# Kernel optimization log

Measured on AMD Instinct MI355X. Metric: run time of the kernel, lower is better.

The kernel has to match this reference:

```python
import jax, jax.numpy as jnp
import numpy as np
from jax import lax

B, T, V, E, H = 256, 16, 32000, 256, 512


def setup_inputs() -> dict:
    key = jax.random.key(0)
    ks = jax.random.split(key, 10)
    s = 0.02
    return {
        "x": jax.random.normal(ks[0], (B, E), dtype=jnp.float32),
        "bb_w": jax.random.normal(ks[1], (H, E), dtype=jnp.float32) * s,
        "bb_b": jnp.zeros((H,), jnp.float32),
        "ln_g": jnp.ones((H,), jnp.float32),
        "ln_b": jnp.zeros((H,), jnp.float32),
        "emb": jax.random.normal(ks[2], (V, E), dtype=jnp.float32) * s,
        "sos": jax.random.normal(ks[3], (E,), dtype=jnp.float32) * 0.01,
        "wih0": jax.random.normal(ks[4], (4 * H, E), dtype=jnp.float32) * s,
        "whh0": jax.random.normal(ks[5], (4 * H, H), dtype=jnp.float32) * s,
        "bih0": jnp.zeros((4 * H,), jnp.float32),
        "bhh0": jnp.zeros((4 * H,), jnp.float32),
        "wih1": jax.random.normal(ks[6], (4 * H, H), dtype=jnp.float32) * s,
        "whh1": jax.random.normal(ks[7], (4 * H, H), dtype=jnp.float32) * s,
        "bih1": jnp.zeros((4 * H,), jnp.float32),
        "bhh1": jnp.zeros((4 * H,), jnp.float32),
        "out_w": jax.random.normal(ks[8], (V, H), dtype=jnp.float32) * s,
        "out_b": jnp.zeros((V,), jnp.float32),
    }


def _lstm_cell(x, h, c, wih, whh, bih, bhh):
    # PyTorch LSTMCell gate order: input, forget, cell(g), output
    g = x @ wih.T + bih + h @ whh.T + bhh
    i, f, gg, o = jnp.split(g, 4, axis=-1)
    c2 = jax.nn.sigmoid(f) * c + jax.nn.sigmoid(i) * jnp.tanh(gg)
    h2 = jax.nn.sigmoid(o) * jnp.tanh(c2)
    return h2, c2


def reference(x, bb_w, bb_b, ln_g, ln_b, emb, sos, wih0, whh0, bih0, bhh0,
              wih1, whh1, bih1, bhh1, out_w, out_b):
    # backbone: Linear -> LayerNorm -> GELU (exact erf, torch default)
    z = x @ bb_w.T + bb_b
    mu = z.mean(-1, keepdims=True)
    var = ((z - mu) ** 2).mean(-1, keepdims=True)
    z = (z - mu) / jnp.sqrt(var + 1e-5) * ln_g + ln_b
    h0 = jax.nn.gelu(z, approximate=False)

    keys = jax.random.split(jax.random.key(1), T)
    init = (
        jnp.broadcast_to(sos[None, :], (B, E)),  # inp
        h0, jnp.zeros_like(h0),                  # layer 0 h, c
        jnp.zeros_like(h0), jnp.zeros_like(h0),  # layer 1 h, c
        jnp.zeros((B,), jnp.bool_),              # done
    )

    def step(carry, key):
        inp, h0_, c0_, h1_, c1_, done = carry
        h0_, c0_ = _lstm_cell(inp, h0_, c0_, wih0, whh0, bih0, bhh0)
        h1_, c1_ = _lstm_cell(h0_, h1_, c1_, wih1, whh1, bih1, bhh1)
        logits = (h1_ @ out_w.T + out_b).astype(jnp.float32)  # [B, V]
        tok = jax.random.categorical(key, logits)
        logl = jax.nn.log_softmax(logits)
        logp = jnp.take_along_axis(logl, tok[:, None], axis=1)[:, 0]
        ent = -jnp.sum(jnp.exp(logl) * logl, axis=-1)
        # varlen masking
        tok = jnp.where(done, 0, tok)
        logp = jnp.where(done, 0.0, logp)
        ent = jnp.where(done, 0.0, ent)
        done = done | (tok == 0)
        inp = emb[tok]
        return (inp, h0_, c0_, h1_, c1_, done), (tok, logp, ent)

    _, (ids, logp, ent) = lax.scan(step, init, keys)
    ids = ids.T          # [B, T]
    logp = logp.T
    ent = ent.T

    # find_lengths_eos + zero ids from (lengths-1) onward
    eos = ids == 0
    has_eos = eos.any(axis=1)
    first = jnp.argmax(eos, axis=1)
    lengths = jnp.where(has_eos, first + 1, T)
    t = jnp.arange(T)[None, :]
    after = t >= (lengths - 1)[:, None]
    ids = jnp.where(after, 0, ids)
    msg = jax.nn.one_hot(ids, V, dtype=jnp.float32)  # [B, T, V]
    return ids, msg, logp, ent, lengths
```

## Files before the change

### kernel.cpp

```cpp
#include <hip/hip_runtime.h>
#include <cstdint>
#include <cmath>

#define B_ 256
#define T_ 16
#define V_ 32000
#define E_ 256
#define H_ 512

typedef __attribute__((ext_vector_type(8))) short bf16x8;
typedef __attribute__((ext_vector_type(4))) float f32x4;

__device__ __forceinline__ uint32_t rotl32(uint32_t x, int r) {
  return (x << r) | (x >> (32 - r));
}

__device__ __forceinline__ void tf2x32(uint32_t k0, uint32_t k1, uint32_t x0, uint32_t x1,
                                       uint32_t& o0, uint32_t& o1) {
  uint32_t k2 = k0 ^ k1 ^ 0x1BD11BDAu;
  x0 += k0; x1 += k1;
#define TFR(r) { x0 += x1; x1 = rotl32(x1, (r)); x1 ^= x0; }
  TFR(13) TFR(15) TFR(26) TFR(6)   x0 += k1; x1 += k2 + 1u;
  TFR(17) TFR(29) TFR(16) TFR(24)  x0 += k2; x1 += k0 + 2u;
  TFR(13) TFR(15) TFR(26) TFR(6)   x0 += k0; x1 += k1 + 3u;
  TFR(17) TFR(29) TFR(16) TFR(24)  x0 += k1; x1 += k2 + 4u;
  TFR(13) TFR(15) TFR(26) TFR(6)   x0 += k2; x1 += k0 + 5u;
#undef TFR
  o0 = x0; o1 = x1;
}

__device__ __forceinline__ uint32_t f2bf(float x) {
  uint32_t u = __float_as_uint(x);
  return (u + 0x7fffu + ((u >> 16) & 1u)) >> 16;
}

typedef const __attribute__((address_space(1))) void* as1_t;
typedef __attribute__((address_space(3))) void* as3_t;
__device__ __forceinline__ void glds16(const void* g, void* l) {
  __builtin_amdgcn_global_load_lds((as1_t)g, (as3_t)l, 16, 0, 0);
}

__global__ __launch_bounds__(256) void prepW3_kernel(
    const float* __restrict__ wih, const float* __restrict__ whh,
    const float* __restrict__ bih, const float* __restrict__ bhh,
    ushort* __restrict__ W3, float* __restrict__ bq, int E, uint32_t* __restrict__ keys)
{
  const int K = E + 512;
  const long long tot = 2048LL * K;
  const long long stride = (long long)gridDim.x * blockDim.x;
  const long long i0 = (long long)blockIdx.x * blockDim.x + threadIdx.x;
  if (keys && i0 < 16) {
    uint32_t o0, o1;
    tf2x32(0u, 1u, 0u, (uint32_t)i0, o0, o1);
    keys[2 * i0] = o0; keys[2 * i0 + 1] = o1;
  }
  for (long long i = i0; i < tot + 2048; i += stride) {
    if (i < tot) {
      int n = (int)(i / K), k = (int)(i % K);
      int j = n >> 2, g = n & 3;
      int r = g * 512 + j;
      float x = (k < E) ? wih[(size_t)r * E + k] : whh[(size_t)r * 512 + (k - E)];
      uint32_t hi = f2bf(x);
      float hf = __uint_as_float(hi << 16);
      uint32_t lo = f2bf(x - hf);
      ushort* row = W3 + (size_t)n * 2 * K;
      row[k] = (ushort)hi;
      row[K + k] = (ushort)lo;
    } else {
      int n = (int)(i - tot);
      int j = n >> 2, g = n & 3;
      bq[n] = bih[g * 512 + j] + bhh[g * 512 + j];
    }
  }
}

__global__ __launch_bounds__(256) void prepB2_kernel(const float* __restrict__ w,
                                                     ushort* __restrict__ B2)
{
  const long long stride = (long long)gridDim.x * blockDim.x;
  for (long long i = (long long)blockIdx.x * blockDim.x + threadIdx.x;
       i < (long long)V_ * 512; i += stride) {
    int n = (int)(i >> 9), k = (int)(i & 511);
    float x = w[i];
    uint32_t hi = f2bf(x);
    float hf = __uint_as_float(hi << 16);
    uint32_t lo = f2bf(x - hf);
    ushort* row = B2 + (size_t)n * 1024;
    row[k] = (ushort)hi;
    row[512 + k] = (ushort)lo;
  }
}

__global__ __launch_bounds__(256) void backbone_kernel(
    const float* __restrict__ x, const float* __restrict__ bb_w, const float* __restrict__ bb_b,
    const float* __restrict__ ln_g, const float* __restrict__ ln_b, const float* __restrict__ sos,
    ushort* __restrict__ A0a, ushort* __restrict__ A1a,
    float* __restrict__ c0, float* __restrict__ c1, int* __restrict__ done)
{
  const int b = blockIdx.x, tid = threadIdx.x;
  __shared__ float xs[E_];
  __shared__ float zs[H_];
  __shared__ float red[256];
  xs[tid] = x[b * E_ + tid];
  __syncthreads();
  for (int jj = 0; jj < 2; ++jj) {
    int j = jj * 256 + tid;
    float acc = 0.0f;
#pragma unroll 4
    for (int k = 0; k < E_; ++k) acc = fmaf(xs[k], bb_w[(size_t)j * E_ + k], acc);
    zs[j] = acc + bb_b[j];
  }
  __syncthreads();
  red[tid] = zs[tid] + zs[tid + 256];
  __syncthreads();
  for (int off = 128; off > 0; off >>= 1) { if (tid < off) red[tid] += red[tid + off]; __syncthreads(); }
  const float mu = red[0] / 512.0f;
  __syncthreads();
  {
    float d0 = zs[tid] - mu, d1 = zs[tid + 256] - mu;
    red[tid] = d0 * d0 + d1 * d1;
  }
  __syncthreads();
  for (int off = 128; off > 0; off >>= 1) { if (tid < off) red[tid] += red[tid + off]; __syncthreads(); }
  const float var = red[0] / 512.0f;
  const float sv = sqrtf(var + 1e-5f);
  for (int jj = 0; jj < 2; ++jj) {
    int j = jj * 256 + tid;
    float zn = (zs[j] - mu) / sv * ln_g[j] + ln_b[j];
    float h = 0.5f * zn * (1.0f + erff(zn / 1.41421356237309515f));
    uint32_t hi = f2bf(h);
    float hf = __uint_as_float(hi << 16);
    uint32_t lo = f2bf(h - hf);
    A0a[(size_t)b * 1536 + 256 + j]  = (ushort)hi;
    A0a[(size_t)b * 1536 + 1024 + j] = (ushort)lo;
    A1a[(size_t)b * 2048 + 512 + j]  = 0;
    A1a[(size_t)b * 2048 + 1536 + j] = 0;
    c0[(size_t)b * 512 + j] = 0.0f;
    c1[(size_t)b * 512 + j] = 0.0f;
  }
  {
    const float xv = sos[tid];
    uint32_t hi = f2bf(xv);
    float hf = __uint_as_float(hi << 16);
    uint32_t lo = f2bf(xv - hf);
    A0a[(size_t)b * 1536 + tid]       = (ushort)hi;
    A0a[(size_t)b * 1536 + 768 + tid] = (ushort)lo;
  }
  if (tid == 0) done[b] = 0;
}

template<int TK>
__global__ __launch_bounds__(256) void mfma_lstm(
    const ushort* __restrict__ A3, const ushort* __restrict__ W3,
    const float* __restrict__ bias, float* __restrict__ c,
    ushort* __restrict__ d1, int rs1, int o1h, int o1l,
    ushort* __restrict__ d2, int rs2, int o2h, int o2l)
{
  constexpr int K = TK * 64;
  constexpr int KC = 3 * TK;
  constexpr int NR = KC / 4;
  constexpr int RS = 2 * K;
  __shared__ __align__(16) char smem[98304];
  const int tid = threadIdx.x;
  const int lane = tid & 63;
  const int wid = tid >> 6;
  const int wm = wid >> 1, wn = wid & 1;
  const int m0 = blockIdx.y * 32;
  const int n0 = blockIdx.x * 64;

  auto stage_chunk = [&](int kc, char* cbase) {
    const int tI = kc / TK;
    const int kin = kc - tI * TK;
    const int abase = (tI == 2 ? K : 0) + kin * 64;
    const int wbase = (tI == 1 ? K : 0) + kin * 64;
    {
      const int o = wid * 1024 + lane * 16;
      const int row = o >> 7;
      const int kb = (o >> 4) & 7;
      glds16(A3 + (size_t)(m0 + row) * RS + abase + ((kb ^ (row & 7)) << 3),
             (void*)(cbase + wid * 1024));
    }
#pragma unroll
    for (int s = 0; s < 2; ++s) {
      const int o = (wid * 2 + s) * 1024 + lane * 16;
      const int row = o >> 7;
      const int kb = (o >> 4) & 7;
      glds16(W3 + (size_t)(n0 + row) * RS + wbase + ((kb ^ (row & 7)) << 3),
             (void*)(cbase + 4096 + (wid * 2 + s) * 1024));
    }
  };
  auto stage_round = [&](int r, char* base) {
#pragma unroll
    for (int cch = 0; cch < 4; ++cch) stage_chunk(r * 4 + cch, base + cch * 12288);
  };

  f32x4 acc[2];
#pragma unroll
  for (int j = 0; j < 2; ++j)
#pragma unroll
    for (int q = 0; q < 4; ++q) acc[j][q] = 0.0f;

  stage_round(0, smem);
  asm volatile("s_waitcnt vmcnt(0)" ::: "memory");
  __syncthreads();
  for (int r = 0; r < NR; ++r) {
    char* cur = smem + (r & 1) * 49152;
    if (r + 1 < NR) stage_round(r + 1, smem + ((r + 1) & 1) * 49152);
#pragma unroll
    for (int cch = 0; cch < 4; ++cch) {
      char* lds = cur + cch * 12288;
#pragma unroll
      for (int ks = 0; ks < 2; ++ks) {
        const int kb = ks * 4 + (lane >> 4);
        const int arow = wm * 16 + (lane & 15);
        bf16x8 a = *(const bf16x8*)(lds + arow * 128 + ((kb ^ (arow & 7)) << 4));
        bf16x8 w[2];
#pragma unroll
        for (int j = 0; j < 2; ++j) {
          const int col = wn * 32 + j * 16 + (lane & 15);
          w[j] = *(const bf16x8*)(lds + 4096 + col * 128 + ((kb ^ (col & 7)) << 4));
        }
#pragma unroll
        for (int j = 0; j < 2; ++j)
          acc[j] = __builtin_amdgcn_mfma_f32_16x16x32_bf16(a, w[j], acc[j], 0, 0, 0);
      }
    }
    asm volatile("s_waitcnt vmcnt(0)" ::: "memory");
    __syncthreads();
  }
  float* gls = (float*)smem;
#pragma unroll
  for (int j = 0; j < 2; ++j)
#pragma unroll
    for (int q = 0; q < 4; ++q)
      gls[(wm * 16 + (lane >> 4) * 4 + q) * 65 + wn * 32 + j * 16 + (lane & 15)] = acc[j][q];
  __syncthreads();
  const int row = tid >> 3;
  const int m = m0 + row;
#pragma unroll
  for (int e = 0; e < 2; ++e) {
    const int ul = (tid & 7) * 2 + e;
    const int nc = ul * 4;
    const float gi = gls[row * 65 + nc + 0] + bias[n0 + nc + 0];
    const float gf = gls[row * 65 + nc + 1] + bias[n0 + nc + 1];
    const float gg = gls[row * 65 + nc + 2] + bias[n0 + nc + 2];
    const float go = gls[row * 65 + nc + 3] + bias[n0 + nc + 3];
    const int u = (n0 >> 2) + ul;
    const float si = 1.0f / (1.0f + expf(-gi));
    const float sf = 1.0f / (1.0f + expf(-gf));
    const float so = 1.0f / (1.0f + expf(-go));
    const float cn = sf * c[(size_t)m * 512 + u] + si * tanhf(gg);
    const float hn = so * tanhf(cn);
    c[(size_t)m * 512 + u] = cn;
    const uint32_t hi = f2bf(hn);
    const float hf = __uint_as_float(hi << 16);
    const uint32_t lo = f2bf(hn - hf);
    d1[(size_t)m * rs1 + o1h + u] = (ushort)hi;
    d1[(size_t)m * rs1 + o1l + u] = (ushort)lo;
    d2[(size_t)m * rs2 + o2h + u] = (ushort)hi;
    d2[(size_t)m * rs2 + o2l + u] = (ushort)lo;
  }
}

__global__ __launch_bounds__(256) void mfma_logits(
    const ushort* __restrict__ A2,
    const ushort* __restrict__ B2,
    const float* __restrict__ bias,
    float* __restrict__ logits)
{
  __shared__ __align__(16) char smem[65536];
  char* lds = smem;
  const int tid = threadIdx.x;
  const int lane = tid & 63;
  const int wid = tid >> 6;
  const int wm = wid >> 1, wn = wid & 1;
  const int bid = blockIdx.x;
  const int xcd = bid & 7, idx = bid >> 3;
  const int wg = (xcd < 4 ? xcd * 63 : 252 + (xcd - 4) * 62) + idx;
  const int m0 = (wg & 1) * 128;
  const int n0 = (wg >> 1) * 128;

  auto stage = [&](int kc, int base) {
    const int tI = kc >> 3;
    const int kin = kc & 7;
    const int abase = (tI == 2 ? 512 : 0) + kin * 64;
    const int bbase = (tI == 1 ? 512 : 0) + kin * 64;
#pragma unroll
    for (int s = 0; s < 4; ++s) {
      const int o = (wid * 4 + s) * 1024 + lane * 16;
      const int row = o >> 7;
      const int kb = (o >> 4) & 7;
      const int sw = (kb ^ (row & 7)) << 3;
      glds16(A2 + (size_t)(m0 + row) * 1024 + abase + sw,
             (void*)(lds + base + (wid * 4 + s) * 1024));
      glds16(B2 + (size_t)(n0 + row) * 1024 + bbase + sw,
             (void*)(lds + base + 16384 + (wid * 4 + s) * 1024));
    }
  };

  f32x4 acc[4][4];
#pragma unroll
  for (int i = 0; i < 4; ++i)
#pragma unroll
    for (int j = 0; j < 4; ++j)
#pragma unroll
      for (int q = 0; q < 4; ++q) acc[i][j][q] = 0.0f;

  stage(0, 0);
  asm volatile("s_waitcnt vmcnt(0)" ::: "memory");
  __syncthreads();
  for (int kc = 0; kc < 24; ++kc) {
    const int cb = (kc & 1) * 32768;
    if (kc + 1 < 24) stage(kc + 1, cb ^ 32768);
#pragma unroll
    for (int ks = 0; ks < 2; ++ks) {
      bf16x8 a[4], b[4];
      const int kb = ks * 4 + (lane >> 4);
#pragma unroll
      for (int i = 0; i < 4; ++i) {
        const int row = wm * 64 + i * 16 + (lane & 15);
        a[i] = *(const bf16x8*)(lds + cb + row * 128 + ((kb ^ (row & 7)) << 4));
        const int col = wn * 64 + i * 16 + (lane & 15);
        b[i] = *(const bf16x8*)(lds + cb + 16384 + col * 128 + ((kb ^ (col & 7)) << 4));
      }
#pragma unroll
      for (int i = 0; i < 4; ++i)
#pragma unroll
        for (int j = 0; j < 4; ++j)
          acc[i][j] = __builtin_amdgcn_mfma_f32_16x16x32_bf16(a[i], b[j], acc[i][j], 0, 0, 0);
    }
    asm volatile("s_waitcnt vmcnt(0)" ::: "memory");
    __syncthreads();
  }
  float bj[4];
#pragma unroll
  for (int j = 0; j < 4; ++j) bj[j] = bias[n0 + wn * 64 + j * 16 + (lane & 15)];
  const int rbase = (lane >> 4) * 4;
#pragma unroll
  for (int i = 0; i < 4; ++i) {
    const int m = m0 + wm * 64 + i * 16 + rbase;
#pragma unroll
    for (int j = 0; j < 4; ++j) {
      const int n = n0 + wn * 64 + j * 16 + (lane & 15);
#pragma unroll
      for (int q = 0; q < 4; ++q)
        logits[(size_t)(m + q) * V_ + n] = acc[i][j][q] + bj[j];
    }
  }
}

__global__ __launch_bounds__(512) void sample_row(
    const float* __restrict__ logits, const uint32_t* __restrict__ keys, int t,
    const float* __restrict__ emb, int* __restrict__ done,
    ushort* __restrict__ A0next, float* __restrict__ ids,
    float* __restrict__ logp, float* __restrict__ ent, float* __restrict__ lens)
{
  const int b = blockIdx.x, tid = threadIdx.x;
  const uint32_t k0 = keys[2 * t], k1 = keys[2 * t + 1];
  const float* lrow = logits + (size_t)b * V_;

  float S = 0.0f, Aa = 0.0f, sb = -INFINITY, lb = 0.0f; int ib = 0;
  float th = -INFINITY;
  int it = 0;
  for (int idx = tid; idx < V_ / 4; idx += 512, ++it) {
    float4 l4 = *(const float4*)&lrow[idx * 4];
    const float le[4] = {l4.x, l4.y, l4.z, l4.w};
#pragma unroll
    for (int e = 0; e < 4; ++e) {
      const int v = idx * 4 + e;
      uint32_t o0, o1;
      tf2x32(k0, k1, 0u, (uint32_t)(b * V_ + v), o0, o1);
      const uint32_t man = (o0 ^ o1) >> 9;
      const float u = (man == 0u) ? 1.17549435e-38f
                                  : __uint_as_float(man | 0x3f800000u) - 1.0f;
      const float ex = expf(le[e]);
      S += ex; Aa = fmaf(ex, le[e], Aa);
      const float thl = fmaxf(th, sb);
      bool need = true;
      if (thl > -1e30f) {
        const float uth = __expf(-__expf(-(thl - le[e] - 1e-3f)));
        need = (u >= uth);
      }
      if (need) {
        const float inner = (float)log((double)u);
        const float outer = (float)log((double)(-inner));
        const float s = le[e] - outer;
        if (s > sb) { sb = s; ib = v; lb = le[e]; }
      }
    }
    if (it == 0 || it == 3) {
      float m2 = sb;
#pragma unroll
      for (int o = 1; o < 64; o <<= 1) m2 = fmaxf(m2, __shfl_xor(m2, o));
      th = m2;
    }
  }
  __shared__ float ss[512], sa[512], sv[512], sl[512];
  __shared__ int si[512];
  ss[tid] = S; sa[tid] = Aa; sv[tid] = sb; si[tid] = ib; sl[tid] = lb;
  __syncthreads();
  for (int o = 256; o > 0; o >>= 1) {
    if (tid < o) {
      ss[tid] += ss[tid + o]; sa[tid] += sa[tid + o];
      float v2 = sv[tid + o]; int i2 = si[tid + o];
      if (v2 > sv[tid] || (v2 == sv[tid] && i2 < si[tid])) {
        sv[tid] = v2; si[tid] = i2; sl[tid] = sl[tid + o];
      }
    }
    __syncthreads();
  }
  if (tid == 0) {
    const float Ssum = ss[0], Asum = sa[0];
    const float logS = logf(Ssum);
    const int tok = si[0];
    const float lp = sl[0] - logS;
    const float en = logS - Asum / Ssum;
    const int dn = done[b];
    const int tokm = dn ? 0 : tok;
    ids[b * T_ + t]  = (float)tokm;
    logp[b * T_ + t] = dn ? 0.0f : lp;
    ent[b * T_ + t]  = dn ? 0.0f : en;
    done[b] = dn | (tokm == 0);
    si[0] = tokm;
    if (t == T_ - 1) {
      int len = T_; bool has = false;
      for (int tt = 0; tt < T_; ++tt) {
        if (!has && ids[b * T_ + tt] == 0.0f) { has = true; len = tt + 1; }
      }
      for (int tt = len - 1; tt < T_; ++tt) ids[b * T_ + tt] = 0.0f;
      lens[b] = (float)len;
    }
  }
  __syncthreads();
  const int tk = si[0];
  if (tid < E_) {
    const float xv = emb[(size_t)tk * E_ + tid];
    const uint32_t hi = f2bf(xv);
    const float hf = __uint_as_float(hi << 16);
    const uint32_t lo = f2bf(xv - hf);
    A0next[(size_t)b * 1536 + tid]       = (ushort)hi;
    A0next[(size_t)b * 1536 + 768 + tid] = (ushort)lo;
  }
}

__global__ __launch_bounds__(256) void msg_kernel(const float* __restrict__ ids,
                                                  float* __restrict__ msg) {
  const int bt = blockIdx.x;
  const int id = (int)ids[bt];
  float4* dst = (float4*)(msg + (size_t)bt * V_);
  for (int q = threadIdx.x; q < V_ / 4; q += 256) {
    const int v = q * 4;
    float4 val;
    val.x = (v     == id) ? 1.0f : 0.0f;
    val.y = (v + 1 == id) ? 1.0f : 0.0f;
    val.z = (v + 2 == id) ? 1.0f : 0.0f;
    val.w = (v + 3 == id) ? 1.0f : 0.0f;
    dst[q] = val;
  }
}

extern "C" void kernel_launch(void* const* d_in, const int* in_sizes, int n_in,
                              void* d_out, int out_size, void* d_ws, size_t ws_size,
                              hipStream_t stream) {
  const float* x    = (const float*)d_in[0];
  const float* bb_w = (const float*)d_in[1];
  const float* bb_b = (const float*)d_in[2];
  const float* ln_g = (const float*)d_in[3];
  const float* ln_b = (const float*)d_in[4];
  const float* emb  = (const float*)d_in[5];
  const float* sos  = (const float*)d_in[6];
  const float* wih0 = (const float*)d_in[7];
  const float* whh0 = (const float*)d_in[8];
  const float* bih0 = (const float*)d_in[9];
  const float* bhh0 = (const float*)d_in[10];
  const float* wih1 = (const float*)d_in[11];
  const float* whh1 = (const float*)d_in[12];
  const float* bih1 = (const float*)d_in[13];
  const float* bhh1 = (const float*)d_in[14];
  const float* out_w = (const float*)d_in[15];
  const float* out_b = (const float*)d_in[16];

  float* out  = (float*)d_out;
  float* ids  = out;
  float* msg  = out + 4096;
  float* logp = out + 131076096;
  float* ent  = out + 131080192;
  float* lens = out + 131084288;

  float* p = msg;
  ushort* W30 = (ushort*)p; p += 1572864;
  ushort* W31 = (ushort*)p; p += 2097152;
  float* bq0 = p; p += 2048;
  float* bq1 = p; p += 2048;
  ushort* A0a = (ushort*)p; p += 196608;
  ushort* A0b = (ushort*)p; p += 196608;
  ushort* A1a = (ushort*)p; p += 262144;
  ushort* A1b = (ushort*)p; p += 262144;
  float* c0 = p; p += 131072;
  float* c1 = p; p += 131072;
  ushort* A2 = (ushort*)p; p += 131072;
  ushort* B2 = (ushort*)p; p += 16384000;
  float* logits = p; p += 8192000;
  uint32_t* keys = (uint32_t*)p; p += 64;
  int* done = (int*)p; p += 256;

  prepW3_kernel<<<2048, 256, 0, stream>>>(wih0, whh0, bih0, bhh0, W30, bq0, 256, keys);
  prepW3_kernel<<<2048, 256, 0, stream>>>(wih1, whh1, bih1, bhh1, W31, bq1, 512, nullptr);
  prepB2_kernel<<<4096, 256, 0, stream>>>(out_w, B2);
  backbone_kernel<<<256, 256, 0, stream>>>(x, bb_w, bb_b, ln_g, ln_b, sos,
                                           A0a, A1a, c0, c1, done);
  for (int t = 0; t < T_; ++t) {
    ushort* A0c = (t & 1) ? A0b : A0a;
    ushort* A0n = (t & 1) ? A0a : A0b;
    ushort* A1c = (t & 1) ? A1b : A1a;
    ushort* A1n = (t & 1) ? A1a : A1b;
    mfma_lstm<12><<<dim3(32, 8), 256, 0, stream>>>(
        A0c, W30, bq0, c0,
        A1c, 2048, 0, 1024,
        A0n, 1536, 256, 1024);
    mfma_lstm<16><<<dim3(32, 8), 256, 0, stream>>>(
        A1c, W31, bq1, c1,
        A1n, 2048, 512, 1536,
        A2, 1024, 0, 512);
    mfma_logits<<<500, 256, 0, stream>>>(A2, B2, out_b, logits);
    sample_row<<<256, 512, 0, stream>>>(logits, keys, t, emb, done,
                                        A0n, ids, logp, ent, lens);
  }
  msg_kernel<<<4096, 256, 0, stream>>>(ids, msg);
}
```

Before: 1.799 ms.

## Fuse Gumbel sampling and softmax stats into logits GEMM epilogue with partial merge

The logits GEMM epilogue now computes per-64-column partial softmax sums, entropy accumulators and Gumbel-max argmax directly from the accumulators, instead of writing the full [B,V] logits tensor. A small merge kernel then reduces the 500 partials per row and does the token bookkeeping and embedding lookup. This removes the large logits write and re-read each step and the separate heavy sampling pass. The cost is extra Threefry and log work in the GEMM epilogue, which adds register pressure, plus an extra partials buffer.

```diff
diff --git a/kernel.cpp b/kernel.cpp
--- a/kernel.cpp
+++ b/kernel.cpp
@@ -262,11 +262,12 @@
   }
 }
 
-__global__ __launch_bounds__(256) void mfma_logits(
+__global__ __launch_bounds__(256) void mfma_sample(
     const ushort* __restrict__ A2,
     const ushort* __restrict__ B2,
     const float* __restrict__ bias,
-    float* __restrict__ logits)
+    const uint32_t* __restrict__ keys, int t,
+    float* __restrict__ partials)
 {
   __shared__ __align__(16) char smem[65536];
   char* lds = smem;
@@ -332,74 +333,102 @@
     asm volatile("s_waitcnt vmcnt(0)" ::: "memory");
     __syncthreads();
   }
+
+  const uint32_t k0 = keys[2 * t], k1 = keys[2 * t + 1];
+  const int lsub = lane & 15;
   float bj[4];
 #pragma unroll
-  for (int j = 0; j < 4; ++j) bj[j] = bias[n0 + wn * 64 + j * 16 + (lane & 15)];
-  const int rbase = (lane >> 4) * 4;
+  for (int j = 0; j < 4; ++j) bj[j] = bias[n0 + wn * 64 + j * 16 + lsub];
+  const int pidx = (n0 >> 6) + wn;
 #pragma unroll
   for (int i = 0; i < 4; ++i) {
-    const int m = m0 + wm * 64 + i * 16 + rbase;
-#pragma unroll
-    for (int j = 0; j < 4; ++j) {
-      const int n = n0 + wn * 64 + j * 16 + (lane & 15);
-#pragma unroll
-      for (int q = 0; q < 4; ++q)
-        logits[(size_t)(m + q) * V_ + n] = acc[i][j][q] + bj[j];
-    }
-  }
-}
-
-__global__ __launch_bounds__(512) void sample_row(
-    const float* __restrict__ logits, const uint32_t* __restrict__ keys, int t,
-    const float* __restrict__ emb, int* __restrict__ done,
-    ushort* __restrict__ A0next, float* __restrict__ ids,
-    float* __restrict__ logp, float* __restrict__ ent, float* __restrict__ lens)
+#pragma unroll
+    for (int q = 0; q < 4; ++q) {
+      const int m = m0 + wm * 64 + i * 16 + (lane >> 4) * 4 + q;
+      float l[4];
+      float S = 0.0f, Aa = 0.0f;
+#pragma unroll
+      for (int j = 0; j < 4; ++j) {
+        l[j] = acc[i][j][q] + bj[j];
+        const float ex = expf(l[j]);
+        S += ex; Aa = fmaf(ex, l[j], Aa);
+      }
+      float sb; int ib; float lb;
+      {
+        const int v = n0 + wn * 64 + lsub;
+        uint32_t o0, o1;
+        tf2x32(k0, k1, 0u, (uint32_t)(m * V_ + v), o0, o1);
+        const uint32_t man = (o0 ^ o1) >> 9;
+        const float u = (man == 0u) ? 1.17549435e-38f
+                                    : __uint_as_float(man | 0x3f800000u) - 1.0f;
+        const float inner = (float)log((double)u);
+        const float outer = (float)log((double)(-inner));
+        sb = l[0] - outer; ib = v; lb = l[0];
+      }
+      float th = sb;
+#pragma unroll
+      for (int o = 1; o < 16; o <<= 1) th = fmaxf(th, __shfl_xor(th, o, 16));
+#pragma unroll
+      for (int j = 1; j < 4; ++j) {
+        const int v = n0 + wn * 64 + j * 16 + lsub;
+        uint32_t o0, o1;
+        tf2x32(k0, k1, 0u, (uint32_t)(m * V_ + v), o0, o1);
+        const uint32_t man = (o0 ^ o1) >> 9;
+        const float u = (man == 0u) ? 1.17549435e-38f
+                                    : __uint_as_float(man | 0x3f800000u) - 1.0f;
+        const float thl = fmaxf(th, sb);
+        const float uth = __expf(-__expf(-(thl - l[j] - 1e-3f)));
+        if (u >= uth) {
+          const float inner = (float)log((double)u);
+          const float outer = (float)log((double)(-inner));
+          const float s = l[j] - outer;
+          if (s > sb) { sb = s; ib = v; lb = l[j]; }
+        }
+      }
+#pragma unroll
+      for (int o = 1; o < 16; o <<= 1) {
+        S  += __shfl_xor(S, o, 16);
+        Aa += __shfl_xor(Aa, o, 16);
+        float s2 = __shfl_xor(sb, o, 16);
+        int   i2 = __shfl_xor(ib, o, 16);
+        float l2 = __shfl_xor(lb, o, 16);
+        if (s2 > sb || (s2 == sb && i2 < ib)) { sb = s2; ib = i2; lb = l2; }
+      }
+      if (lsub == 0) {
+        float* dst = partials + ((size_t)m * 500 + pidx) * 8;
+        *(float4*)dst = make_float4(S, Aa, sb, __int_as_float(ib));
+        dst[4] = lb;
+      }
+    }
+  }
+}
+
+__global__ __launch_bounds__(256) void merge_sample(
+    const float* __restrict__ partials, const float* __restrict__ emb,
+    int t, int* __restrict__ done, ushort* __restrict__ A0next,
+    float* __restrict__ ids, float* __restrict__ logp, float* __restrict__ ent,
+    float* __restrict__ lens)
 {
   const int b = blockIdx.x, tid = threadIdx.x;
-  const uint32_t k0 = keys[2 * t], k1 = keys[2 * t + 1];
-  const float* lrow = logits + (size_t)b * V_;
-
-  float S = 0.0f, Aa = 0.0f, sb = -INFINITY, lb = 0.0f; int ib = 0;
-  float th = -INFINITY;
-  int it = 0;
-  for (int idx = tid; idx < V_ / 4; idx += 512, ++it) {
-    float4 l4 = *(const float4*)&lrow[idx * 4];
-    const float le[4] = {l4.x, l4.y, l4.z, l4.w};
-#pragma unroll
-    for (int e = 0; e < 4; ++e) {
-      const int v = idx * 4 + e;
-      uint32_t o0, o1;
-      tf2x32(k0, k1, 0u, (uint32_t)(b * V_ + v), o0, o1);
-      const uint32_t man = (o0 ^ o1) >> 9;
-      const float u = (man == 0u) ? 1.17549435e-38f
-                                  : __uint_as_float(man | 0x3f800000u) - 1.0f;
-      const float ex = expf(le[e]);
-      S += ex; Aa = fmaf(ex, le[e], Aa);
-      const float thl = fmaxf(th, sb);
-      bool need = true;
-      if (thl > -1e30f) {
-        const float uth = __expf(-__expf(-(thl - le[e] - 1e-3f)));
-        need = (u >= uth);
-      }
-      if (need) {
-        const float inner = (float)log((double)u);
-        const float outer = (float)log((double)(-inner));
-        const float s = le[e] - outer;
-        if (s > sb) { sb = s; ib = v; lb = le[e]; }
-      }
-    }
-    if (it == 0 || it == 3) {
-      float m2 = sb;
-#pragma unroll
-      for (int o = 1; o < 64; o <<= 1) m2 = fmaxf(m2, __shfl_xor(m2, o));
-      th = m2;
-    }
-  }
-  __shared__ float ss[512], sa[512], sv[512], sl[512];
-  __shared__ int si[512];
+  float S = 0.0f, Aa = 0.0f, sb = -INFINITY, lb = 0.0f;
+  int ib = 0x7fffffff;
+  {
+    const float* src = partials + ((size_t)b * 500 + tid) * 8;
+    float4 p0 = *(const float4*)src;
+    S = p0.x; Aa = p0.y; sb = p0.z; ib = __float_as_int(p0.w); lb = src[4];
+  }
+  if (tid + 256 < 500) {
+    const float* src = partials + ((size_t)b * 500 + tid + 256) * 8;
+    float4 p0 = *(const float4*)src;
+    S += p0.x; Aa += p0.y;
+    float s2 = p0.z; int i2 = __float_as_int(p0.w);
+    if (s2 > sb || (s2 == sb && i2 < ib)) { sb = s2; ib = i2; lb = src[4]; }
+  }
+  __shared__ float ss[256], sa[256], sv[256], sl[256];
+  __shared__ int si[256];
   ss[tid] = S; sa[tid] = Aa; sv[tid] = sb; si[tid] = ib; sl[tid] = lb;
   __syncthreads();
-  for (int o = 256; o > 0; o >>= 1) {
+  for (int o = 128; o > 0; o >>= 1) {
     if (tid < o) {
       ss[tid] += ss[tid + o]; sa[tid] += sa[tid + o];
       float v2 = sv[tid + o]; int i2 = si[tid + o];
@@ -410,11 +439,11 @@
     __syncthreads();
   }
   if (tid == 0) {
-    const float Ssum = ss[0], Asum = sa[0];
-    const float logS = logf(Ssum);
+    const float Sg = ss[0], Ag = sa[0];
+    const float logS = logf(Sg);
     const int tok = si[0];
     const float lp = sl[0] - logS;
-    const float en = logS - Asum / Ssum;
+    const float en = logS - Ag / Sg;
     const int dn = done[b];
     const int tokm = dn ? 0 : tok;
     ids[b * T_ + t]  = (float)tokm;
@@ -433,7 +462,7 @@
   }
   __syncthreads();
   const int tk = si[0];
-  if (tid < E_) {
+  {
     const float xv = emb[(size_t)tk * E_ + tid];
     const uint32_t hi = f2bf(xv);
     const float hf = __uint_as_float(hi << 16);
@@ -500,7 +529,7 @@
   float* c1 = p; p += 131072;
   ushort* A2 = (ushort*)p; p += 131072;
   ushort* B2 = (ushort*)p; p += 16384000;
-  float* logits = p; p += 8192000;
+  float* partials = p; p += 1024000;
   uint32_t* keys = (uint32_t*)p; p += 64;
   int* done = (int*)p; p += 256;
 
@@ -522,9 +551,9 @@
         A1c, W31, bq1, c1,
         A1n, 2048, 512, 1536,
         A2, 1024, 0, 512);
-    mfma_logits<<<500, 256, 0, stream>>>(A2, B2, out_b, logits);
-    sample_row<<<256, 512, 0, stream>>>(logits, keys, t, emb, done,
-                                        A0n, ids, logp, ent, lens);
+    mfma_sample<<<500, 256, 0, stream>>>(A2, B2, out_b, keys, t, partials);
+    merge_sample<<<256, 256, 0, stream>>>(partials, emb, t, done, A0n,
+                                          ids, logp, ent, lens);
   }
   msg_kernel<<<4096, 256, 0, stream>>>(ids, msg);
 }
```

Result: slower. 3.436 ms (+91.0%).

## Merge weight-prep kernels and split logits GEMM tile over eight waves

Applied to the files above, without the earlier changes.

Three weight-preparation launches are folded into one grid-stride kernel, which removes two kernel launches. The logits GEMM block grows from 4 to 8 waves; each wave now covers a 64x32 sub-tile instead of 64x64, and staging is spread across more threads. The goal is more waves per CU to hide LDS and MFMA latency during the 500-block logits GEMM that runs every timestep. The cost is lower MFMA work per A-fragment load, since A is reloaded for only two B columns, and more LDS read traffic per block.

```diff
diff --git a/kernel.cpp b/kernel.cpp
--- a/kernel.cpp
+++ b/kernel.cpp
@@ -40,54 +40,67 @@
   __builtin_amdgcn_global_load_lds((as1_t)g, (as3_t)l, 16, 0, 0);
 }
 
-__global__ __launch_bounds__(256) void prepW3_kernel(
-    const float* __restrict__ wih, const float* __restrict__ whh,
-    const float* __restrict__ bih, const float* __restrict__ bhh,
-    ushort* __restrict__ W3, float* __restrict__ bq, int E, uint32_t* __restrict__ keys)
+__global__ __launch_bounds__(256) void prep_all(
+    const float* __restrict__ wih0, const float* __restrict__ whh0,
+    const float* __restrict__ bih0, const float* __restrict__ bhh0,
+    const float* __restrict__ wih1, const float* __restrict__ whh1,
+    const float* __restrict__ bih1, const float* __restrict__ bhh1,
+    const float* __restrict__ out_w,
+    ushort* __restrict__ W30, ushort* __restrict__ W31,
+    float* __restrict__ bq0, float* __restrict__ bq1,
+    ushort* __restrict__ B2, uint32_t* __restrict__ keys)
 {
-  const int K = E + 512;
-  const long long tot = 2048LL * K;
   const long long stride = (long long)gridDim.x * blockDim.x;
   const long long i0 = (long long)blockIdx.x * blockDim.x + threadIdx.x;
-  if (keys && i0 < 16) {
+  if (i0 < 16) {
     uint32_t o0, o1;
     tf2x32(0u, 1u, 0u, (uint32_t)i0, o0, o1);
     keys[2 * i0] = o0; keys[2 * i0 + 1] = o1;
   }
-  for (long long i = i0; i < tot + 2048; i += stride) {
-    if (i < tot) {
-      int n = (int)(i / K), k = (int)(i % K);
-      int j = n >> 2, g = n & 3;
-      int r = g * 512 + j;
-      float x = (k < E) ? wih[(size_t)r * E + k] : whh[(size_t)r * 512 + (k - E)];
+  const long long S0 = 2048LL * 768;
+  const long long T1 = S0;
+  const long long T2 = T1 + 2048LL * 1024;
+  const long long T3 = T2 + 2048;
+  const long long T4 = T3 + 2048;
+  const long long T5 = T4 + 32000LL * 512;
+  for (long long i = i0; i < T5; i += stride) {
+    if (i < T1) {
+      int n = (int)(i / 768), k = (int)(i % 768);
+      int r = (n & 3) * 512 + (n >> 2);
+      float x = (k < 256) ? wih0[(size_t)r * 256 + k] : whh0[(size_t)r * 512 + (k - 256)];
       uint32_t hi = f2bf(x);
       float hf = __uint_as_float(hi << 16);
       uint32_t lo = f2bf(x - hf);
-      ushort* row = W3 + (size_t)n * 2 * K;
-      row[k] = (ushort)hi;
-      row[K + k] = (ushort)lo;
+      ushort* row = W30 + (size_t)n * 1536;
+      row[k] = (ushort)hi; row[768 + k] = (ushort)lo;
+    } else if (i < T2) {
+      long long q = i - T1;
+      int n = (int)(q / 1024), k = (int)(q % 1024);
+      int r = (n & 3) * 512 + (n >> 2);
+      float x = (k < 512) ? wih1[(size_t)r * 512 + k] : whh1[(size_t)r * 512 + (k - 512)];
+      uint32_t hi = f2bf(x);
+      float hf = __uint_as_float(hi << 16);
+      uint32_t lo = f2bf(x - hf);
+      ushort* row = W31 + (size_t)n * 2048;
+      row[k] = (ushort)hi; row[1024 + k] = (ushort)lo;
+    } else if (i < T3) {
+      int n = (int)(i - T2);
+      int r = (n & 3) * 512 + (n >> 2);
+      bq0[n] = bih0[r] + bhh0[r];
+    } else if (i < T4) {
+      int n = (int)(i - T3);
+      int r = (n & 3) * 512 + (n >> 2);
+      bq1[n] = bih1[r] + bhh1[r];
     } else {
-      int n = (int)(i - tot);
-      int j = n >> 2, g = n & 3;
-      bq[n] = bih[g * 512 + j] + bhh[g * 512 + j];
-    }
-  }
-}
-
-__global__ __launch_bounds__(256) void prepB2_kernel(const float* __restrict__ w,
-                                                     ushort* __restrict__ B2)
-{
-  const long long stride = (long long)gridDim.x * blockDim.x;
-  for (long long i = (long long)blockIdx.x * blockDim.x + threadIdx.x;
-       i < (long long)V_ * 512; i += stride) {
-    int n = (int)(i >> 9), k = (int)(i & 511);
-    float x = w[i];
-    uint32_t hi = f2bf(x);
-    float hf = __uint_as_float(hi << 16);
-    uint32_t lo = f2bf(x - hf);
-    ushort* row = B2 + (size_t)n * 1024;
-    row[k] = (ushort)hi;
-    row[512 + k] = (ushort)lo;
+      long long q = i - T4;
+      int n = (int)(q >> 9), k = (int)(q & 511);
+      float x = out_w[q];
+      uint32_t hi = f2bf(x);
+      float hf = __uint_as_float(hi << 16);
+      uint32_t lo = f2bf(x - hf);
+      ushort* row = B2 + (size_t)n * 1024;
+      row[k] = (ushort)hi; row[512 + k] = (ushort)lo;
+    }
   }
 }
 
@@ -262,7 +275,7 @@
   }
 }
 
-__global__ __launch_bounds__(256) void mfma_logits(
+__global__ __launch_bounds__(512) void mfma_logits(
     const ushort* __restrict__ A2,
     const ushort* __restrict__ B2,
     const float* __restrict__ bias,
@@ -273,7 +286,7 @@
   const int tid = threadIdx.x;
   const int lane = tid & 63;
   const int wid = tid >> 6;
-  const int wm = wid >> 1, wn = wid & 1;
+  const int wm = wid >> 2, wn = wid & 3;
   const int bid = blockIdx.x;
   const int xcd = bid & 7, idx = bid >> 3;
   const int wg = (xcd < 4 ? xcd * 63 : 252 + (xcd - 4) * 62) + idx;
@@ -286,23 +299,23 @@
     const int abase = (tI == 2 ? 512 : 0) + kin * 64;
     const int bbase = (tI == 1 ? 512 : 0) + kin * 64;
 #pragma unroll
-    for (int s = 0; s < 4; ++s) {
-      const int o = (wid * 4 + s) * 1024 + lane * 16;
+    for (int s = 0; s < 2; ++s) {
+      const int o = (wid * 2 + s) * 1024 + lane * 16;
       const int row = o >> 7;
       const int kb = (o >> 4) & 7;
       const int sw = (kb ^ (row & 7)) << 3;
       glds16(A2 + (size_t)(m0 + row) * 1024 + abase + sw,
-             (void*)(lds + base + (wid * 4 + s) * 1024));
+             (void*)(lds + base + (wid * 2 + s) * 1024));
       glds16(B2 + (size_t)(n0 + row) * 1024 + bbase + sw,
-             (void*)(lds + base + 16384 + (wid * 4 + s) * 1024));
+             (void*)(lds + base + 16384 + (wid * 2 + s) * 1024));
     }
   };
 
-  f32x4 acc[4][4];
+  f32x4 acc[4][2];
 #pragma unroll
   for (int i = 0; i < 4; ++i)
 #pragma unroll
-    for (int j = 0; j < 4; ++j)
+    for (int j = 0; j < 2; ++j)
 #pragma unroll
       for (int q = 0; q < 4; ++q) acc[i][j][q] = 0.0f;
 
@@ -314,34 +327,38 @@
     if (kc + 1 < 24) stage(kc + 1, cb ^ 32768);
 #pragma unroll
     for (int ks = 0; ks < 2; ++ks) {
-      bf16x8 a[4], b[4];
+      bf16x8 a[4], b[2];
       const int kb = ks * 4 + (lane >> 4);
 #pragma unroll
       for (int i = 0; i < 4; ++i) {
         const int row = wm * 64 + i * 16 + (lane & 15);
         a[i] = *(const bf16x8*)(lds + cb + row * 128 + ((kb ^ (row & 7)) << 4));
-        const int col = wn * 64 + i * 16 + (lane & 15);
-        b[i] = *(const bf16x8*)(lds + cb + 16384 + col * 128 + ((kb ^ (col & 7)) << 4));
+      }
+#pragma unroll
+      for (int j = 0; j < 2; ++j) {
+        const int col = wn * 32 + j * 16 + (lane & 15);
+        b[j] = *(const bf16x8*)(lds + cb + 16384 + col * 128 + ((kb ^ (col & 7)) << 4));
       }
 #pragma unroll
       for (int i = 0; i < 4; ++i)
 #pragma unroll
-        for (int j = 0; j < 4; ++j)
+        for (int j = 0; j < 2; ++j)
           acc[i][j] = __builtin_amdgcn_mfma_f32_16x16x32_bf16(a[i], b[j], acc[i][j], 0, 0, 0);
     }
     asm volatile("s_waitcnt vmcnt(0)" ::: "memory");
     __syncthreads();
   }
-  float bj[4];
-#pragma unroll
-  for (int j = 0; j < 4; ++j) bj[j] = bias[n0 + wn * 64 + j * 16 + (lane & 15)];
+  const int lsub = lane & 15;
+  float bj[2];
+#pragma unroll
+  for (int j = 0; j < 2; ++j) bj[j] = bias[n0 + wn * 32 + j * 16 + lsub];
   const int rbase = (lane >> 4) * 4;
 #pragma unroll
   for (int i = 0; i < 4; ++i) {
     const int m = m0 + wm * 64 + i * 16 + rbase;
 #pragma unroll
-    for (int j = 0; j < 4; ++j) {
-      const int n = n0 + wn * 64 + j * 16 + (lane & 15);
+    for (int j = 0; j < 2; ++j) {
+      const int n = n0 + wn * 32 + j * 16 + lsub;
 #pragma unroll
       for (int q = 0; q < 4; ++q)
         logits[(size_t)(m + q) * V_ + n] = acc[i][j][q] + bj[j];
@@ -504,9 +521,9 @@
   uint32_t* keys = (uint32_t*)p; p += 64;
   int* done = (int*)p; p += 256;
 
-  prepW3_kernel<<<2048, 256, 0, stream>>>(wih0, whh0, bih0, bhh0, W30, bq0, 256, keys);
-  prepW3_kernel<<<2048, 256, 0, stream>>>(wih1, whh1, bih1, bhh1, W31, bq1, 512, nullptr);
-  prepB2_kernel<<<4096, 256, 0, stream>>>(out_w, B2);
+  prep_all<<<4096, 256, 0, stream>>>(wih0, whh0, bih0, bhh0,
+                                     wih1, whh1, bih1, bhh1, out_w,
+                                     W30, W31, bq0, bq1, B2, keys);
   backbone_kernel<<<256, 256, 0, stream>>>(x, bb_w, bb_b, ln_g, ln_b, sos,
                                            A0a, A1a, c0, c1, done);
   for (int t = 0; t < T_; ++t) {
@@ -522,7 +539,7 @@
         A1c, W31, bq1, c1,
         A1n, 2048, 512, 1536,
         A2, 1024, 0, 512);
-    mfma_logits<<<500, 256, 0, stream>>>(A2, B2, out_b, logits);
+    mfma_logits<<<500, 512, 0, stream>>>(A2, B2, out_b, logits);
     sample_row<<<256, 512, 0, stream>>>(logits, keys, t, emb, done,
                                         A0n, ids, logp, ent, lens);
   }
```

After: 1.787 ms. No clear change (-0.7%).
